# Kernel optimization log

Hardware: AMD Instinct MI355X
Metric: run time of the kernel (lower is better)

The kernel has to match this reference:

```python
import jax, jax.numpy as jnp
import numpy as np

D_MODEL, D_FF, N_EXPERTS, TOP_K = 1024, 4096, 8, 2
BATCH, SEQ = 2, 2048


def setup_inputs() -> dict:
    key = jax.random.key(0)
    ks = jax.random.split(key, 4)
    s_in = 1.0 / np.sqrt(D_MODEL)
    s_ff = 1.0 / np.sqrt(D_FF)
    return {
        "x": jax.random.normal(ks[0], (BATCH, SEQ, D_MODEL), dtype=jnp.float32),
        "Wr": jax.random.normal(ks[1], (D_MODEL, N_EXPERTS), dtype=jnp.float32) * s_in,
        "br": jnp.zeros((N_EXPERTS,), dtype=jnp.float32),
        "W1": jax.random.normal(ks[2], (N_EXPERTS, D_MODEL, D_FF), dtype=jnp.float32) * s_in,
        "b1": jnp.zeros((N_EXPERTS, D_FF), dtype=jnp.float32),
        "W2": jax.random.normal(ks[3], (N_EXPERTS, D_FF, D_MODEL), dtype=jnp.float32) * s_ff,
        "b2": jnp.zeros((N_EXPERTS, D_MODEL), dtype=jnp.float32),
    }


def reference(x, Wr, br, W1, b1, W2, b2):
    B, S, D = x.shape
    E = Wr.shape[1]
    xf = x.reshape(-1, D)  # [T, D]

    # Router: softmax over experts, top-2, renormalize selected weights
    probs = jax.nn.softmax(xf @ Wr + br, axis=-1)            # [T, E]
    top_w, top_i = jax.lax.top_k(probs, TOP_K)               # [T, k]
    top_w = top_w / jnp.sum(top_w, axis=-1, keepdims=True)

    onehot = jax.nn.one_hot(top_i, E, dtype=xf.dtype)        # [T, k, E]
    util = onehot.mean(axis=(0, 1))                          # [E]
    combine = jnp.einsum('tk,tke->te', top_w, onehot)        # [T, E]

    # Grouped expert MLP over all tokens, then weighted combine
    h = jax.nn.gelu(jnp.einsum('td,edf->etf', xf, W1) + b1[:, None, :],
                    approximate=False)                       # [E, T, F]
    y = jnp.einsum('etf,efd->etd', h, W2) + b2[:, None, :]   # [E, T, D]
    out = jnp.einsum('te,etd->td', combine, y).reshape(B, S, D)

    # Aux load-balance loss: squared coefficient of variation (unbiased std)
    cv = jnp.std(util, ddof=1) / (jnp.mean(util) + 1e-6)
    return out, cv ** 2
```

## Files before the change

### kernel.cpp

```cpp
#include <hip/hip_runtime.h>
#include <hip/hip_bf16.h>

#define T_TOK 4096
#define DM 1024
#define DF 4096
#define NE 8

typedef __attribute__((ext_vector_type(4))) float f32x4;
typedef __attribute__((ext_vector_type(8))) short bf16x8;

__device__ inline unsigned short f2bf(float f) {
  union { float f; unsigned u; } a; a.f = f;
  unsigned r = a.u + 0x7fffu + ((a.u >> 16) & 1u);
  return (unsigned short)(r >> 16);
}
__device__ inline unsigned pk(float lo, float hi) {
  return (unsigned)f2bf(lo) | ((unsigned)f2bf(hi) << 16);
}
__device__ inline float bf2f(unsigned short u) {
  union { unsigned u; float f; } a; a.u = ((unsigned)u) << 16; return a.f;
}

__device__ inline void gload16(const void* g, void* l) {
  __builtin_amdgcn_global_load_lds(
      (const __attribute__((address_space(1))) unsigned int*)g,
      (__attribute__((address_space(3))) unsigned int*)l, 16, 0, 0);
}

__global__ __launch_bounds__(256) void k_router(const float* __restrict__ x,
    const float* __restrict__ Wr, const float* __restrict__ br,
    int* __restrict__ topi, float* __restrict__ topw, int* __restrict__ counts) {
  int t = blockIdx.x;
  int tid = threadIdx.x;
  const float* xr = x + (size_t)t * DM;
  float acc[NE];
#pragma unroll
  for (int e = 0; e < NE; e++) acc[e] = 0.f;
  for (int d = tid; d < DM; d += 256) {
    float xv = xr[d];
    const float* w = Wr + (size_t)d * NE;
#pragma unroll
    for (int e = 0; e < NE; e++) acc[e] += xv * w[e];
  }
  __shared__ float red[NE][256];
#pragma unroll
  for (int e = 0; e < NE; e++) red[e][tid] = acc[e];
  __syncthreads();
  for (int s = 128; s > 0; s >>= 1) {
    if (tid < s) {
#pragma unroll
      for (int e = 0; e < NE; e++) red[e][tid] += red[e][tid + s];
    }
    __syncthreads();
  }
  if (tid == 0) {
    float l[NE];
#pragma unroll
    for (int e = 0; e < NE; e++) l[e] = red[e][0] + br[e];
    int i0 = 0;
#pragma unroll
    for (int e = 1; e < NE; e++) if (l[e] > l[i0]) i0 = e;
    int i1 = (i0 == 0) ? 1 : 0;
#pragma unroll
    for (int e = 0; e < NE; e++) if (e != i0 && l[e] > l[i1]) i1 = e;
    float w1e = expf(l[i1] - l[i0]);
    float w0 = 1.f / (1.f + w1e);
    topi[2 * t] = i0; topi[2 * t + 1] = i1;
    topw[2 * t] = w0; topw[2 * t + 1] = w1e * w0;
    atomicAdd(&counts[i0], 1);
    atomicAdd(&counts[i1], 1);
  }
}

__global__ void k_scan(const int* __restrict__ counts, int* __restrict__ offsets,
                       float* __restrict__ cv2out) {
  if (threadIdx.x == 0) {
    int off = 0;
    float util[NE];
    for (int e = 0; e < NE; e++) { offsets[e] = off; off += counts[e]; }
    offsets[NE] = off;
    float mean = 0.f;
    for (int e = 0; e < NE; e++) { util[e] = (float)counts[e] / (float)(2 * T_TOK); mean += util[e]; }
    mean *= (1.f / NE);
    float var = 0.f;
    for (int e = 0; e < NE; e++) { float d = util[e] - mean; var += d * d; }
    var *= (1.f / (NE - 1));
    float den = mean + 1e-6f;
    *cv2out = var / (den * den);
  }
}

__global__ __launch_bounds__(256) void k_scatter(const int* __restrict__ topi,
    const int* __restrict__ offsets, int* __restrict__ cursor,
    int* __restrict__ perm, int* __restrict__ tslot) {
  int t = blockIdx.x * 256 + threadIdx.x;
  if (t >= T_TOK) return;
#pragma unroll
  for (int k = 0; k < 2; k++) {
    int e = topi[2 * t + k];
    int p = atomicAdd(&cursor[e], 1);
    int s = offsets[e] + p;
    perm[s] = t;
    tslot[2 * t + k] = s;
  }
}

__global__ __launch_bounds__(256) void k_cvtx(const float* __restrict__ x,
    unsigned short* __restrict__ xc) {
  size_t i = ((size_t)blockIdx.x * 256 + threadIdx.x) * 8;
  f32x4 a = *(const f32x4*)(x + i);
  f32x4 b = *(const f32x4*)(x + i + 4);
  uint4 v;
  v.x = pk(a[0], a[1]); v.y = pk(a[2], a[3]);
  v.z = pk(b[0], b[1]); v.w = pk(b[2], b[3]);
  *(uint4*)(xc + i) = v;
}

__global__ __launch_bounds__(256) void k_cvtT(const float* __restrict__ src,
    unsigned short* __restrict__ dst, int K, int N) {
  int e = blockIdx.z;
  int n0 = blockIdx.x * 64, k0 = blockIdx.y * 64;
  int tid = threadIdx.x;
  __shared__ float tile[64][65];
  const float* s = src + (size_t)e * K * N + (size_t)k0 * N + n0;
  int r0 = tid >> 4, c4 = (tid & 15) * 4;
#pragma unroll
  for (int i = 0; i < 4; i++) {
    int r = r0 + i * 16;
    float4 v = *(const float4*)(s + (size_t)r * N + c4);
    tile[r][c4] = v.x; tile[r][c4 + 1] = v.y; tile[r][c4 + 2] = v.z; tile[r][c4 + 3] = v.w;
  }
  __syncthreads();
  int n = tid >> 2, kc = (tid & 3) * 16;
  unsigned o[8];
#pragma unroll
  for (int j = 0; j < 8; j++)
    o[j] = pk(tile[kc + 2 * j][n], tile[kc + 2 * j + 1][n]);
  unsigned short* dp = dst + (size_t)e * N * K + (size_t)(n0 + n) * K + k0 + kc;
  *(uint4*)dp = make_uint4(o[0], o[1], o[2], o[3]);
  *(uint4*)(dp + 8) = make_uint4(o[4], o[5], o[6], o[7]);
}


__global__ __launch_bounds__(256) void k_gemm1(const unsigned short* __restrict__ xc,
    const unsigned short* __restrict__ W1t, const float* __restrict__ b1,
    const int* __restrict__ offsets, const int* __restrict__ perm,
    unsigned short* __restrict__ hb) {
  int e = blockIdx.z;
  int roff = offsets[e];
  int nrows = offsets[e + 1] - roff;
  int row_base = blockIdx.y * 128;
  if (row_base >= nrows) return;
  int n0 = blockIdx.x * 128;
  int tid = threadIdx.x, lane = tid & 63, wid = tid >> 6;
  int wm = (wid >> 1) * 64, wn = (wid & 1) * 64;

  __shared__ __align__(16) unsigned short smA[2][128 * 64];
  __shared__ __align__(16) unsigned short smB[2][128 * 64];
  __shared__ int tok_s[128];
  if (tid < 128) {
    int r = row_base + tid;
    tok_s[tid] = (r < nrows) ? perm[roff + r] : 0;
  }
  __syncthreads();

  f32x4 acc[4][4];
#pragma unroll
  for (int m = 0; m < 4; m++)
#pragma unroll
    for (int n = 0; n < 4; n++) acc[m][n] = (f32x4)(0.f);

  const unsigned short* Bbase = W1t + (size_t)e * DF * DM + (size_t)n0 * DM;

  const unsigned short* aP[4];
  const unsigned short* bP[4];
  int ldsOff[4];
#pragma unroll
  for (int i = 0; i < 4; i++) {
    int c = tid + i * 256;
    int row = c >> 3;
    int o = ((c & 7) ^ (row & 7)) * 8;
    aP[i] = xc + (size_t)tok_s[row] * DM + o;
    bP[i] = Bbase + (size_t)row * DM + o;
    ldsOff[i] = c * 8;
  }
  int rA[2][4], rB[2][4];
#pragma unroll
  for (int ks = 0; ks < 2; ks++) {
#pragma unroll
    for (int m = 0; m < 4; m++) {
      int rowa = wm + m * 16 + (lane & 15);
      int rowb = wn + m * 16 + (lane & 15);
      int col = ks * 64 + (lane >> 4) * 16;
      rA[ks][m] = rowa * 128 + (col ^ ((rowa & 7) << 4));
      rB[ks][m] = rowb * 128 + (col ^ ((rowb & 7) << 4));
    }
  }

#define STAGE1(kk, p)                                        \
  {                                                          \
    int k0_ = (kk) * 64;                                     \
    _Pragma("unroll")                                        \
    for (int i = 0; i < 4; i++) {                            \
      gload16(aP[i] + k0_, &smA[p][ldsOff[i]]);              \
      gload16(bP[i] + k0_, &smB[p][ldsOff[i]]);              \
    }                                                        \
  }
#define COMPUTE1(p)                                                            \
  {                                                                            \
    const char* A_ = (const char*)smA[p];                                      \
    const char* B_ = (const char*)smB[p];                                      \
    _Pragma("unroll")                                                          \
    for (int ks = 0; ks < 2; ks++) {                                           \
      bf16x8 af[4], bfr[4];                                                    \
      _Pragma("unroll")                                                        \
      for (int m = 0; m < 4; m++) af[m] = *(const bf16x8*)(A_ + rA[ks][m]);    \
      _Pragma("unroll")                                                        \
      for (int n = 0; n < 4; n++) bfr[n] = *(const bf16x8*)(B_ + rB[ks][n]);   \
      _Pragma("unroll")                                                        \
      for (int m = 0; m < 4; m++)                                              \
        _Pragma("unroll")                                                      \
        for (int n = 0; n < 4; n++)                                            \
          acc[m][n] = __builtin_amdgcn_mfma_f32_16x16x32_bf16(af[m], bfr[n],   \
                                                              acc[m][n], 0, 0, 0); \
    }                                                                          \
  }

  STAGE1(0, 0);
  for (int t = 0; t < DM / 64 - 1; ++t) {
    STAGE1(t + 1, (t + 1) & 1);
    asm volatile("s_waitcnt vmcnt(8)" ::: "memory");
    __builtin_amdgcn_s_barrier();
    __builtin_amdgcn_sched_barrier(0);
    COMPUTE1(t & 1);
    asm volatile("s_waitcnt lgkmcnt(0)" ::: "memory");
    __builtin_amdgcn_sched_barrier(0);
    __builtin_amdgcn_s_barrier();
  }
  asm volatile("s_waitcnt vmcnt(0)" ::: "memory");
  __builtin_amdgcn_s_barrier();
  __builtin_amdgcn_sched_barrier(0);
  COMPUTE1((DM / 64 - 1) & 1);

#pragma unroll
  for (int n = 0; n < 4; n++) {
    int col = n0 + wn + n * 16 + (lane & 15);
    float b1v = b1[e * DF + col];
#pragma unroll
    for (int m = 0; m < 4; m++) {
      int rbase = wm + m * 16 + ((lane >> 4) << 2);
#pragma unroll
      for (int r = 0; r < 4; r++) {
        int grow = row_base + rbase + r;
        if (grow < nrows) {
          float v = acc[m][n][r] + b1v;
          float g = 0.5f * v * (1.f + erff(v * 0.70710678118f));
          hb[(size_t)(roff + grow) * DF + col] = f2bf(g);
        }
      }
    }
  }
}

__global__ __launch_bounds__(256) void k_gemm2(const unsigned short* __restrict__ hb,
    const unsigned short* __restrict__ W2t, const int* __restrict__ offsets,
    unsigned short* __restrict__ y) {
  int e = blockIdx.z;
  int roff = offsets[e];
  int nrows = offsets[e + 1] - roff;
  int row_base = blockIdx.y * 128;
  if (row_base >= nrows) return;
  int n0 = blockIdx.x * 128;
  int tid = threadIdx.x, lane = tid & 63, wid = tid >> 6;
  int wm = (wid >> 1) * 64, wn = (wid & 1) * 64;

  __shared__ __align__(16) unsigned short smA[2][128 * 64];
  __shared__ __align__(16) unsigned short smB[2][128 * 64];

  f32x4 acc[4][4];
#pragma unroll
  for (int m = 0; m < 4; m++)
#pragma unroll
    for (int n = 0; n < 4; n++) acc[m][n] = (f32x4)(0.f);

  const unsigned short* Abase = hb + (size_t)(roff + row_base) * DF;
  const unsigned short* Bbase = W2t + (size_t)e * DM * DF + (size_t)n0 * DF;

  const unsigned short* aP[4];
  const unsigned short* bP[4];
  int ldsOff[4];
#pragma unroll
  for (int i = 0; i < 4; i++) {
    int c = tid + i * 256;
    int row = c >> 3;
    int o = ((c & 7) ^ (row & 7)) * 8;
    aP[i] = Abase + (size_t)row * DF + o;
    bP[i] = Bbase + (size_t)row * DF + o;
    ldsOff[i] = c * 8;
  }
  int rA[2][4], rB[2][4];
#pragma unroll
  for (int ks = 0; ks < 2; ks++) {
#pragma unroll
    for (int m = 0; m < 4; m++) {
      int rowa = wm + m * 16 + (lane & 15);
      int rowb = wn + m * 16 + (lane & 15);
      int col = ks * 64 + (lane >> 4) * 16;
      rA[ks][m] = rowa * 128 + (col ^ ((rowa & 7) << 4));
      rB[ks][m] = rowb * 128 + (col ^ ((rowb & 7) << 4));
    }
  }

#define STAGE2(kk, p)                                        \
  {                                                          \
    int k0_ = (kk) * 64;                                     \
    _Pragma("unroll")                                        \
    for (int i = 0; i < 4; i++) {                            \
      gload16(aP[i] + k0_, &smA[p][ldsOff[i]]);              \
      gload16(bP[i] + k0_, &smB[p][ldsOff[i]]);              \
    }                                                        \
  }
#define COMPUTE2(p)                                                            \
  {                                                                            \
    const char* A_ = (const char*)smA[p];                                      \
    const char* B_ = (const char*)smB[p];                                      \
    _Pragma("unroll")                                                          \
    for (int ks = 0; ks < 2; ks++) {                                           \
      bf16x8 af[4], bfr[4];                                                    \
      _Pragma("unroll")                                                        \
      for (int m = 0; m < 4; m++) af[m] = *(const bf16x8*)(A_ + rA[ks][m]);    \
      _Pragma("unroll")                                                        \
      for (int n = 0; n < 4; n++) bfr[n] = *(const bf16x8*)(B_ + rB[ks][n]);   \
      _Pragma("unroll")                                                        \
      for (int m = 0; m < 4; m++)                                              \
        _Pragma("unroll")                                                      \
        for (int n = 0; n < 4; n++)                                            \
          acc[m][n] = __builtin_amdgcn_mfma_f32_16x16x32_bf16(af[m], bfr[n],   \
                                                              acc[m][n], 0, 0, 0); \
    }                                                                          \
  }

  STAGE2(0, 0);
  for (int t = 0; t < DF / 64 - 1; ++t) {
    STAGE2(t + 1, (t + 1) & 1);
    asm volatile("s_waitcnt vmcnt(8)" ::: "memory");
    __builtin_amdgcn_s_barrier();
    __builtin_amdgcn_sched_barrier(0);
    COMPUTE2(t & 1);
    asm volatile("s_waitcnt lgkmcnt(0)" ::: "memory");
    __builtin_amdgcn_sched_barrier(0);
    __builtin_amdgcn_s_barrier();
  }
  asm volatile("s_waitcnt vmcnt(0)" ::: "memory");
  __builtin_amdgcn_s_barrier();
  __builtin_amdgcn_sched_barrier(0);
  COMPUTE2((DF / 64 - 1) & 1);

#pragma unroll
  for (int m = 0; m < 4; m++) {
    int rbase = wm + m * 16 + ((lane >> 4) << 2);
#pragma unroll
    for (int r = 0; r < 4; r++) {
      int grow = row_base + rbase + r;
      if (grow < nrows) {
#pragma unroll
        for (int n = 0; n < 4; n++) {
          int col = n0 + wn + n * 16 + (lane & 15);
          y[(size_t)(roff + grow) * DM + col] = f2bf(acc[m][n][r]);
        }
      }
    }
  }
}

__global__ __launch_bounds__(256) void k_combine(const int* __restrict__ topi,
    const float* __restrict__ topw, const int* __restrict__ tslot,
    const unsigned short* __restrict__ y, const float* __restrict__ b2,
    float* __restrict__ out) {
  int t = blockIdx.x, tid = threadIdx.x;
  int s0 = tslot[2 * t], s1 = tslot[2 * t + 1];
  int e0 = topi[2 * t], e1 = topi[2 * t + 1];
  float w0 = topw[2 * t], w1 = topw[2 * t + 1];
  int d = tid * 4;
  uint2 ya = *(const uint2*)(y + (size_t)s0 * DM + d);
  uint2 yb = *(const uint2*)(y + (size_t)s1 * DM + d);
  f32x4 bb0 = *(const f32x4*)(b2 + (size_t)e0 * DM + d);
  f32x4 bb1 = *(const f32x4*)(b2 + (size_t)e1 * DM + d);
  f32x4 r;
  r[0] = w0 * (bf2f((unsigned short)(ya.x & 0xffff)) + bb0[0]) + w1 * (bf2f((unsigned short)(yb.x & 0xffff)) + bb1[0]);
  r[1] = w0 * (bf2f((unsigned short)(ya.x >> 16)) + bb0[1]) + w1 * (bf2f((unsigned short)(yb.x >> 16)) + bb1[1]);
  r[2] = w0 * (bf2f((unsigned short)(ya.y & 0xffff)) + bb0[2]) + w1 * (bf2f((unsigned short)(yb.y & 0xffff)) + bb1[2]);
  r[3] = w0 * (bf2f((unsigned short)(ya.y >> 16)) + bb0[3]) + w1 * (bf2f((unsigned short)(yb.y >> 16)) + bb1[3]);
  *(f32x4*)(out + (size_t)t * DM + d) = r;
}

extern "C" void kernel_launch(void* const* d_in, const int* in_sizes, int n_in,
                              void* d_out, int out_size, void* d_ws, size_t ws_size,
                              hipStream_t stream) {
  const float* x  = (const float*)d_in[0];
  const float* Wr = (const float*)d_in[1];
  const float* br = (const float*)d_in[2];
  const float* W1 = (const float*)d_in[3];
  const float* b1 = (const float*)d_in[4];
  const float* W2 = (const float*)d_in[5];
  const float* b2 = (const float*)d_in[6];
  float* out = (float*)d_out;

  char* ws = (char*)d_ws;
  int*   counts  = (int*)(ws + 0);
  int*   cursor  = (int*)(ws + 64);
  int*   offsets = (int*)(ws + 128);
  int*   topi    = (int*)(ws + 256);
  float* topw    = (float*)(ws + 33024);
  int*   perm    = (int*)(ws + 65792);
  int*   tslot   = (int*)(ws + 98560);
  unsigned short* xc  = (unsigned short*)(ws + 164096);
  unsigned short* hb  = (unsigned short*)(ws + 8552704);
  unsigned short* y   = (unsigned short*)(ws + 75661568);
  unsigned short* W1t = (unsigned short*)(ws + 92438784);
  unsigned short* W2t = (unsigned short*)(ws + 159547648);

  hipMemsetAsync(ws, 0, 256, stream);

  k_cvtx<<<T_TOK * DM / (256 * 8), 256, 0, stream>>>(x, xc);
  k_cvtT<<<dim3(DF / 64, DM / 64, NE), 256, 0, stream>>>(W1, W1t, DM, DF);
  k_cvtT<<<dim3(DM / 64, DF / 64, NE), 256, 0, stream>>>(W2, W2t, DF, DM);
  k_router<<<T_TOK, 256, 0, stream>>>(x, Wr, br, topi, topw, counts);
  k_scan<<<1, 64, 0, stream>>>(counts, offsets, out + (size_t)T_TOK * DM);
  k_scatter<<<16, 256, 0, stream>>>(topi, offsets, cursor, perm, tslot);
  k_gemm1<<<dim3(32, 32, 8), 256, 0, stream>>>(xc, W1t, b1, offsets, perm, hb);
  k_gemm2<<<dim3(8, 32, 8), 256, 0, stream>>>(hb, W2t, offsets, y);
  k_combine<<<T_TOK, 256, 0, stream>>>(topi, topw, tslot, y, b2, out);
}
```

Before: 799.5 us.

## Enlarge GEMM tiles to 256-wide with 512-thread blocks and cheaper GELU

Both expert GEMMs move to 512-thread blocks with larger output tiles (256x256 for the first, 128x256 for the second), raising data reuse per LDS load and halving global traffic for weights and activations. The hand-tuned waitcnt/barrier pipeline is replaced by plain __syncthreads, which simplifies sync but may serialize loads and compute. The erf-based GELU is replaced by a sigmoid/tanh-form approximation using a fast exp, cutting epilogue cost at a small accuracy cost. The larger tiles use more LDS and registers and may reduce occupancy.

```diff
diff --git a/kernel.cpp b/kernel.cpp
--- a/kernel.cpp
+++ b/kernel.cpp
@@ -19,6 +19,10 @@
 }
 __device__ inline float bf2f(unsigned short u) {
   union { unsigned u; float f; } a; a.u = ((unsigned)u) << 16; return a.f;
+}
+__device__ inline float gelu_f(float v) {
+  float u = 1.5957691216f * v * (1.f + 0.044715f * v * v);
+  return v / (1.f + __expf(-u));
 }
 
 __device__ inline void gload16(const void* g, void* l) {
@@ -142,31 +146,31 @@
 }
 
 
-__global__ __launch_bounds__(256) void k_gemm1(const unsigned short* __restrict__ xc,
+__global__ __launch_bounds__(512) void k_gemm1(const unsigned short* __restrict__ xc,
     const unsigned short* __restrict__ W1t, const float* __restrict__ b1,
     const int* __restrict__ offsets, const int* __restrict__ perm,
     unsigned short* __restrict__ hb) {
   int e = blockIdx.z;
   int roff = offsets[e];
   int nrows = offsets[e + 1] - roff;
-  int row_base = blockIdx.y * 128;
+  int row_base = blockIdx.y * 256;
   if (row_base >= nrows) return;
-  int n0 = blockIdx.x * 128;
+  int n0 = blockIdx.x * 256;
   int tid = threadIdx.x, lane = tid & 63, wid = tid >> 6;
-  int wm = (wid >> 1) * 64, wn = (wid & 1) * 64;
-
-  __shared__ __align__(16) unsigned short smA[2][128 * 64];
-  __shared__ __align__(16) unsigned short smB[2][128 * 64];
-  __shared__ int tok_s[128];
-  if (tid < 128) {
+  int wr = wid >> 2, wc = wid & 3;
+
+  __shared__ __align__(16) unsigned short smA[2][256 * 64];
+  __shared__ __align__(16) unsigned short smB[2][256 * 64];
+  __shared__ int tok_s[256];
+  if (tid < 256) {
     int r = row_base + tid;
     tok_s[tid] = (r < nrows) ? perm[roff + r] : 0;
   }
   __syncthreads();
 
-  f32x4 acc[4][4];
-#pragma unroll
-  for (int m = 0; m < 4; m++)
+  f32x4 acc[8][4];
+#pragma unroll
+  for (int m = 0; m < 8; m++)
 #pragma unroll
     for (int n = 0; n < 4; n++) acc[m][n] = (f32x4)(0.f);
 
@@ -177,23 +181,26 @@
   int ldsOff[4];
 #pragma unroll
   for (int i = 0; i < 4; i++) {
-    int c = tid + i * 256;
+    int c = tid + i * 512;
     int row = c >> 3;
     int o = ((c & 7) ^ (row & 7)) * 8;
     aP[i] = xc + (size_t)tok_s[row] * DM + o;
     bP[i] = Bbase + (size_t)row * DM + o;
     ldsOff[i] = c * 8;
   }
-  int rA[2][4], rB[2][4];
+  int rA[2][8], rB[2][4];
 #pragma unroll
   for (int ks = 0; ks < 2; ks++) {
-#pragma unroll
-    for (int m = 0; m < 4; m++) {
-      int rowa = wm + m * 16 + (lane & 15);
-      int rowb = wn + m * 16 + (lane & 15);
-      int col = ks * 64 + (lane >> 4) * 16;
-      rA[ks][m] = rowa * 128 + (col ^ ((rowa & 7) << 4));
-      rB[ks][m] = rowb * 128 + (col ^ ((rowb & 7) << 4));
+    int colb = ks * 64 + (lane >> 4) * 16;
+#pragma unroll
+    for (int m = 0; m < 8; m++) {
+      int row = wr * 128 + m * 16 + (lane & 15);
+      rA[ks][m] = row * 128 + (colb ^ ((row & 7) << 4));
+    }
+#pragma unroll
+    for (int n = 0; n < 4; n++) {
+      int row = wc * 64 + n * 16 + (lane & 15);
+      rB[ks][n] = row * 128 + (colb ^ ((row & 7) << 4));
     }
   }
 
@@ -212,13 +219,13 @@
     const char* B_ = (const char*)smB[p];                                      \
     _Pragma("unroll")                                                          \
     for (int ks = 0; ks < 2; ks++) {                                           \
-      bf16x8 af[4], bfr[4];                                                    \
-      _Pragma("unroll")                                                        \
-      for (int m = 0; m < 4; m++) af[m] = *(const bf16x8*)(A_ + rA[ks][m]);    \
+      bf16x8 af[8], bfr[4];                                                    \
+      _Pragma("unroll")                                                        \
+      for (int m = 0; m < 8; m++) af[m] = *(const bf16x8*)(A_ + rA[ks][m]);    \
       _Pragma("unroll")                                                        \
       for (int n = 0; n < 4; n++) bfr[n] = *(const bf16x8*)(B_ + rB[ks][n]);   \
       _Pragma("unroll")                                                        \
-      for (int m = 0; m < 4; m++)                                              \
+      for (int m = 0; m < 8; m++)                                              \
         _Pragma("unroll")                                                      \
         for (int n = 0; n < 4; n++)                                            \
           acc[m][n] = __builtin_amdgcn_mfma_f32_16x16x32_bf16(af[m], bfr[n],   \
@@ -227,42 +234,32 @@
   }
 
   STAGE1(0, 0);
+  __syncthreads();
   for (int t = 0; t < DM / 64 - 1; ++t) {
     STAGE1(t + 1, (t + 1) & 1);
-    asm volatile("s_waitcnt vmcnt(8)" ::: "memory");
-    __builtin_amdgcn_s_barrier();
-    __builtin_amdgcn_sched_barrier(0);
     COMPUTE1(t & 1);
-    asm volatile("s_waitcnt lgkmcnt(0)" ::: "memory");
-    __builtin_amdgcn_sched_barrier(0);
-    __builtin_amdgcn_s_barrier();
-  }
-  asm volatile("s_waitcnt vmcnt(0)" ::: "memory");
-  __builtin_amdgcn_s_barrier();
-  __builtin_amdgcn_sched_barrier(0);
+    __syncthreads();
+  }
   COMPUTE1((DM / 64 - 1) & 1);
 
 #pragma unroll
   for (int n = 0; n < 4; n++) {
-    int col = n0 + wn + n * 16 + (lane & 15);
+    int col = n0 + wc * 64 + n * 16 + (lane & 15);
     float b1v = b1[e * DF + col];
 #pragma unroll
-    for (int m = 0; m < 4; m++) {
-      int rbase = wm + m * 16 + ((lane >> 4) << 2);
+    for (int m = 0; m < 8; m++) {
+      int rbase = wr * 128 + m * 16 + ((lane >> 4) << 2);
 #pragma unroll
       for (int r = 0; r < 4; r++) {
         int grow = row_base + rbase + r;
-        if (grow < nrows) {
-          float v = acc[m][n][r] + b1v;
-          float g = 0.5f * v * (1.f + erff(v * 0.70710678118f));
-          hb[(size_t)(roff + grow) * DF + col] = f2bf(g);
-        }
+        if (grow < nrows)
+          hb[(size_t)(roff + grow) * DF + col] = f2bf(gelu_f(acc[m][n][r] + b1v));
       }
     }
   }
 }
 
-__global__ __launch_bounds__(256) void k_gemm2(const unsigned short* __restrict__ hb,
+__global__ __launch_bounds__(512) void k_gemm2(const unsigned short* __restrict__ hb,
     const unsigned short* __restrict__ W2t, const int* __restrict__ offsets,
     unsigned short* __restrict__ y) {
   int e = blockIdx.z;
@@ -270,12 +267,12 @@
   int nrows = offsets[e + 1] - roff;
   int row_base = blockIdx.y * 128;
   if (row_base >= nrows) return;
-  int n0 = blockIdx.x * 128;
+  int n0 = blockIdx.x * 256;
   int tid = threadIdx.x, lane = tid & 63, wid = tid >> 6;
-  int wm = (wid >> 1) * 64, wn = (wid & 1) * 64;
+  int wr = wid >> 2, wc = wid & 3;
 
   __shared__ __align__(16) unsigned short smA[2][128 * 64];
-  __shared__ __align__(16) unsigned short smB[2][128 * 64];
+  __shared__ __align__(16) unsigned short smB[2][256 * 64];
 
   f32x4 acc[4][4];
 #pragma unroll
@@ -286,28 +283,36 @@
   const unsigned short* Abase = hb + (size_t)(roff + row_base) * DF;
   const unsigned short* Bbase = W2t + (size_t)e * DM * DF + (size_t)n0 * DF;
 
-  const unsigned short* aP[4];
+  const unsigned short* aP[2];
+  int aOff[2];
   const unsigned short* bP[4];
-  int ldsOff[4];
-#pragma unroll
-  for (int i = 0; i < 4; i++) {
-    int c = tid + i * 256;
+  int bOff[4];
+#pragma unroll
+  for (int i = 0; i < 2; i++) {
+    int c = tid + i * 512;
     int row = c >> 3;
     int o = ((c & 7) ^ (row & 7)) * 8;
     aP[i] = Abase + (size_t)row * DF + o;
+    aOff[i] = c * 8;
+  }
+#pragma unroll
+  for (int i = 0; i < 4; i++) {
+    int c = tid + i * 512;
+    int row = c >> 3;
+    int o = ((c & 7) ^ (row & 7)) * 8;
     bP[i] = Bbase + (size_t)row * DF + o;
-    ldsOff[i] = c * 8;
+    bOff[i] = c * 8;
   }
   int rA[2][4], rB[2][4];
 #pragma unroll
   for (int ks = 0; ks < 2; ks++) {
+    int colb = ks * 64 + (lane >> 4) * 16;
 #pragma unroll
     for (int m = 0; m < 4; m++) {
-      int rowa = wm + m * 16 + (lane & 15);
-      int rowb = wn + m * 16 + (lane & 15);
-      int col = ks * 64 + (lane >> 4) * 16;
-      rA[ks][m] = rowa * 128 + (col ^ ((rowa & 7) << 4));
-      rB[ks][m] = rowb * 128 + (col ^ ((rowb & 7) << 4));
+      int rowa = wr * 64 + m * 16 + (lane & 15);
+      int rowb = wc * 64 + m * 16 + (lane & 15);
+      rA[ks][m] = rowa * 128 + (colb ^ ((rowa & 7) << 4));
+      rB[ks][m] = rowb * 128 + (colb ^ ((rowb & 7) << 4));
     }
   }
 
@@ -315,10 +320,11 @@
   {                                                          \
     int k0_ = (kk) * 64;                                     \
     _Pragma("unroll")                                        \
-    for (int i = 0; i < 4; i++) {                            \
-      gload16(aP[i] + k0_, &smA[p][ldsOff[i]]);              \
-      gload16(bP[i] + k0_, &smB[p][ldsOff[i]]);              \
-    }                                                        \
+    for (int i = 0; i < 2; i++)                              \
+      gload16(aP[i] + k0_, &smA[p][aOff[i]]);                \
+    _Pragma("unroll")                                        \
+    for (int i = 0; i < 4; i++)                              \
+      gload16(bP[i] + k0_, &smB[p][bOff[i]]);                \
   }
 #define COMPUTE2(p)                                                            \
   {                                                                            \
@@ -341,31 +347,24 @@
   }
 
   STAGE2(0, 0);
+  __syncthreads();
   for (int t = 0; t < DF / 64 - 1; ++t) {
     STAGE2(t + 1, (t + 1) & 1);
-    asm volatile("s_waitcnt vmcnt(8)" ::: "memory");
-    __builtin_amdgcn_s_barrier();
-    __builtin_amdgcn_sched_barrier(0);
     COMPUTE2(t & 1);
-    asm volatile("s_waitcnt lgkmcnt(0)" ::: "memory");
-    __builtin_amdgcn_sched_barrier(0);
-    __builtin_amdgcn_s_barrier();
-  }
-  asm volatile("s_waitcnt vmcnt(0)" ::: "memory");
-  __builtin_amdgcn_s_barrier();
-  __builtin_amdgcn_sched_barrier(0);
+    __syncthreads();
+  }
   COMPUTE2((DF / 64 - 1) & 1);
 
 #pragma unroll
   for (int m = 0; m < 4; m++) {
-    int rbase = wm + m * 16 + ((lane >> 4) << 2);
+    int rbase = wr * 64 + m * 16 + ((lane >> 4) << 2);
 #pragma unroll
     for (int r = 0; r < 4; r++) {
       int grow = row_base + rbase + r;
       if (grow < nrows) {
 #pragma unroll
         for (int n = 0; n < 4; n++) {
-          int col = n0 + wn + n * 16 + (lane & 15);
+          int col = n0 + wc * 64 + n * 16 + (lane & 15);
           y[(size_t)(roff + grow) * DM + col] = f2bf(acc[m][n][r]);
         }
       }
@@ -428,7 +427,7 @@
   k_router<<<T_TOK, 256, 0, stream>>>(x, Wr, br, topi, topw, counts);
   k_scan<<<1, 64, 0, stream>>>(counts, offsets, out + (size_t)T_TOK * DM);
   k_scatter<<<16, 256, 0, stream>>>(topi, offsets, cursor, perm, tslot);
-  k_gemm1<<<dim3(32, 32, 8), 256, 0, stream>>>(xc, W1t, b1, offsets, perm, hb);
-  k_gemm2<<<dim3(8, 32, 8), 256, 0, stream>>>(hb, W2t, offsets, y);
+  k_gemm1<<<dim3(16, 16, 8), 512, 0, stream>>>(xc, W1t, b1, offsets, perm, hb);
+  k_gemm2<<<dim3(4, 32, 8), 512, 0, stream>>>(hb, W2t, offsets, y);
   k_combine<<<T_TOK, 256, 0, stream>>>(topi, topw, tslot, y, b2, out);
 }
```

New measurement: 814.7 us. No clear change (+1.9%).
